# Performance work log

Hardware: AMD Instinct MI355X
Metric: run time of the kernel (lower is better)

The kernel has to match this reference:

```python
import jax, jax.numpy as jnp
import numpy as np

D = 32        # number of TT cores (d)
R = 16        # tt_rank
B = 262144    # batch size


def setup_inputs() -> dict:
    key = jax.random.key(0)
    k1, k2, k3, k4 = jax.random.split(key, 4)
    return {
        "X": jax.random.randint(k1, (B, D), 0, 2, dtype=jnp.int32),
        "core_first": jax.random.normal(k2, (1, R, 2), dtype=jnp.float32),
        "cores_mid": jax.random.normal(k3, (D - 2, R, R, 2), dtype=jnp.float32),
        "core_last": jax.random.normal(k4, (R, 1, 2), dtype=jnp.float32),
    }


def reference(X, core_first, cores_mid, core_last):
    # First core: cores[0][:, :, X[:,0]] -> [1, R, B] -> permute -> [B, 1, R].
    # We carry the squeezed [B, R] row vector instead of [B, 1, R].
    carry0 = jnp.take(core_first[0], X[:, 0], axis=-1).T  # [B, R]

    def step(carry, inp):
        core, idx = inp                       # core: [R, R, 2], idx: [B]
        c = jnp.take(core, idx, axis=2)       # gathered core: [R, R, B]
        new = jnp.einsum('br,rsb->bs', carry, c)  # batched (1xR)@(RxR)
        return new, None

    # Middle cores i = 1 .. D-2 (sequential chain, data-dependent).
    carry, _ = jax.lax.scan(step, carry0, (cores_mid, X[:, 1:D - 1].T))

    # Last core: cores[-1][:, :, X[:,-1]] -> [R, 1, B]; contract to scalar per batch.
    c_last = jnp.take(core_last[:, 0, :], X[:, -1], axis=-1)  # [R, B]
    out = jnp.einsum('br,rb->b', carry, c_last)               # [B]  (squeeze of [B,1,1])
    return out
```

## Files before the change

### kernel.cpp

```cpp
#include <hip/hip_runtime.h>


#define R 16
#define TT_D 32
#define BATCH 262144

#define OFF_V16  0
#define OFF_W16  1048576
#define OFF_P8   2097152
#define OFF_Q8   (OFF_P8 + 65536)
#define OFF_V8   (OFF_Q8 + 65536)
#define OFF_W8   (OFF_V8 + 4096)
#define OFF_PK   (OFF_W8 + 4096)
#define WS_FLOATS (OFF_PK + BATCH)

#define NBLK1 1024
#define NTAB  34

__device__ __forceinline__ void rowvec_mat(const float* __restrict__ M,
                                           float* __restrict__ u) {
    float nv[R];
    #pragma unroll
    for (int s = 0; s < R; s++) nv[s] = 0.f;
    #pragma unroll
    for (int t2 = 0; t2 < R; t2++) {
        const float a = u[t2];
        #pragma unroll
        for (int s = 0; s < R; s++) nv[s] += a * M[t2 * 16 + s];
    }
    #pragma unroll
    for (int s = 0; s < R; s++) u[s] = nv[s];
}

__device__ __forceinline__ void mat_colvec(const float* __restrict__ M,
                                           float* __restrict__ w) {
    float nw[R];
    #pragma unroll
    for (int r2 = 0; r2 < R; r2++) {
        float a = 0.f;
        #pragma unroll
        for (int k = 0; k < R; k++) a += M[r2 * 16 + k] * w[k];
        nw[r2] = a;
    }
    #pragma unroll
    for (int r2 = 0; r2 < R; r2++) w[r2] = nw[r2];
}

__global__ __launch_bounds__(256) void tt_stage1(const int* __restrict__ X,
                                                 const float* __restrict__ cf,
                                                 const float* __restrict__ cm,
                                                 const float* __restrict__ cl,
                                                 float* __restrict__ ws) {
    __shared__ float scm[8 * 512];
    const int blk = blockIdx.x;
    const int t = threadIdx.x;

    if (blk < NTAB) {
        int cbase, ncore;
        if (blk < 16)       { cbase = 7;  ncore = 8; }
        else if (blk < 32)  { cbase = 15; ncore = 8; }
        else if (blk == 32) { cbase = 0;  ncore = 7; }
        else                { cbase = 23; ncore = 7; }
        const float2* cm2 = (const float2*)(cm + cbase * 512);
        for (int j = t; j < ncore * 256; j += 256) {
            const float2 vv = cm2[j];
            const int ci = j >> 8, idx = j & 255;
            scm[ci * 512 + idx] = vv.x;
            scm[ci * 512 + 256 + idx] = vv.y;
        }
        __syncthreads();

        if (blk < 32) {
            const bool isP = (blk < 16);
            const int e = (isP ? blk : blk - 16) * 16 + (t >> 4), r = t & 15;
            float u[R];
            const float* M0 = scm + ((e >> 7) & 1) * 256;
            #pragma unroll
            for (int s = 0; s < R; s++) u[s] = M0[r * 16 + s];
            for (int k = 1; k < 8; k++)
                rowvec_mat(scm + k * 512 + ((e >> (7 - k)) & 1) * 256, u);
            float* o = ws + (isP ? OFF_P8 : OFF_Q8) + e * 256 + r * 16;
            #pragma unroll
            for (int s = 0; s < R; s++) o[s] = u[s];
        } else if (blk == 32) {
            const int e = t;
            float u[R];
            #pragma unroll
            for (int s = 0; s < R; s++) u[s] = cf[s * 2 + ((e >> 7) & 1)];
            for (int k = 0; k < 7; k++)
                rowvec_mat(scm + k * 512 + ((e >> (6 - k)) & 1) * 256, u);
            float* o = ws + OFF_V8 + e * 16;
            #pragma unroll
            for (int s = 0; s < R; s++) o[s] = u[s];
        } else {
            const int e = t;
            float w[R];
            #pragma unroll
            for (int r2 = 0; r2 < R; r2++) w[r2] = cl[r2 * 2 + (e & 1)];
            for (int j = 6; j >= 0; j--)
                mat_colvec(scm + j * 512 + ((e >> (7 - j)) & 1) * 256, w);
            float* o = ws + OFF_W8 + e * 16;
            #pragma unroll
            for (int r2 = 0; r2 < R; r2++) o[r2] = w[r2];
        }
    } else {
        unsigned* pk = (unsigned*)(ws + OFF_PK);
        const int stride = (NBLK1 - NTAB) * 256;
        for (int b = (blk - NTAB) * 256 + t; b < BATCH; b += stride) {
            const int4* Xr = (const int4*)(X + (size_t)b * TT_D);
            unsigned p = 0, s = 0;
            #pragma unroll
            for (int q = 0; q < 4; q++) {
                const int4 c = Xr[q];
                p = (p << 4) | ((unsigned)(c.x & 1) << 3) | ((unsigned)(c.y & 1) << 2)
                             | ((unsigned)(c.z & 1) << 1) | (unsigned)(c.w & 1);
            }
            #pragma unroll
            for (int q = 4; q < 8; q++) {
                const int4 c = Xr[q];
                s = (s << 4) | ((unsigned)(c.x & 1) << 3) | ((unsigned)(c.y & 1) << 2)
                             | ((unsigned)(c.z & 1) << 1) | (unsigned)(c.w & 1);
            }
            pk[b] = (p << 16) | s;
        }
    }
}

__global__ __launch_bounds__(256) void tt_stage2(float* __restrict__ ws) {
    __shared__ float sQ[256];
    const int blk = blockIdx.x;
    const int t = threadIdx.x;
    if (blk < 256) {
        const int hi = blk, lo = t;
        float u[R];
        const float* v8 = ws + OFF_V8 + hi * 16;
        #pragma unroll
        for (int k = 0; k < R; k++) u[k] = v8[k];
        rowvec_mat(ws + OFF_P8 + lo * 256, u);
        float* o = ws + OFF_V16 + (size_t)(hi * 256 + lo) * 16;
        #pragma unroll
        for (int s = 0; s < R; s++) o[s] = u[s];
    } else {
        const int hi = blk - 256, lo = t;
        sQ[t] = ws[OFF_Q8 + hi * 256 + t];
        __syncthreads();
        float w[R];
        const float* w8 = ws + OFF_W8 + lo * 16;
        #pragma unroll
        for (int k = 0; k < R; k++) w[k] = w8[k];
        mat_colvec(sQ, w);
        float* o = ws + OFF_W16 + (size_t)(hi * 256 + lo) * 16;
        #pragma unroll
        for (int r2 = 0; r2 < R; r2++) o[r2] = w[r2];
    }
}

__global__ __launch_bounds__(256) void tt_gather(const float* __restrict__ ws,
                                                 float* __restrict__ out) {
    const int b = blockIdx.x * 256 + threadIdx.x;
    const unsigned pk = ((const unsigned*)(ws + OFF_PK))[b];
    const unsigned p = pk >> 16, s = pk & 0xffffu;
    const float4* v = (const float4*)(ws + OFF_V16 + (size_t)p * 16);
    const float4* w = (const float4*)(ws + OFF_W16 + (size_t)s * 16);
    float acc = 0.f;
    #pragma unroll
    for (int k = 0; k < 4; k++) {
        const float4 a = v[k], c = w[k];
        acc += a.x * c.x + a.y * c.y + a.z * c.z + a.w * c.w;
    }
    out[b] = acc;
}

__global__ __launch_bounds__(256) void tt_direct(const int* __restrict__ X,
                                                 const float* __restrict__ cf,
                                                 const float* __restrict__ cm,
                                                 const float* __restrict__ cl,
                                                 float* __restrict__ out) {
    __shared__ float scm[30 * 16 * 16 * 2];
    for (int i = threadIdx.x; i < 30 * 16 * 16 * 2; i += blockDim.x) scm[i] = cm[i];
    __syncthreads();
    const int b = blockIdx.x * blockDim.x + threadIdx.x;
    if (b >= BATCH) return;
    const int* xr = X + (size_t)b * TT_D;
    float v[R], nv[R];
    const int x0 = xr[0] & 1;
    #pragma unroll
    for (int rr = 0; rr < R; rr++) v[rr] = cf[rr * 2 + x0];
    for (int i = 1; i <= 30; i++) {
        const int bit = xr[i] & 1;
        const float* M = scm + (i - 1) * 512;
        #pragma unroll
        for (int s2 = 0; s2 < R; s2++) {
            float acc = 0.f;
            #pragma unroll
            for (int rr = 0; rr < R; rr++) acc += v[rr] * M[(rr * 16 + s2) * 2 + bit];
            nv[s2] = acc;
        }
        #pragma unroll
        for (int s2 = 0; s2 < R; s2++) v[s2] = nv[s2];
    }
    const int xl = xr[31] & 1;
    float acc = 0.f;
    #pragma unroll
    for (int rr = 0; rr < R; rr++) acc += v[rr] * cl[rr * 2 + xl];
    out[b] = acc;
}

extern "C" void kernel_launch(void* const* d_in, const int* in_sizes, int n_in,
                              void* d_out, int out_size, void* d_ws, size_t ws_size,
                              hipStream_t stream) {
    const int* X = (const int*)d_in[0];
    const float* cf = (const float*)d_in[1];
    const float* cm = (const float*)d_in[2];
    const float* cl = (const float*)d_in[3];
    float* out = (float*)d_out;

    if (ws_size >= (size_t)WS_FLOATS * sizeof(float)) {
        float* ws = (float*)d_ws;
        tt_stage1<<<NBLK1, 256, 0, stream>>>(X, cf, cm, cl, ws);
        tt_stage2<<<512, 256, 0, stream>>>(ws);
        tt_gather<<<BATCH / 256, 256, 0, stream>>>(ws, out);
    } else {
        tt_direct<<<(BATCH + 255) / 256, 256, 0, stream>>>(X, cf, cm, cl, out);
    }
}
```

Baseline: 117.4 us.

## Replace three-kernel prefix/suffix table scheme with single direct per-row chain kernel

Removes the meet-in-the-middle scheme that built 65536-entry prefix and suffix tables, along with its stage kernels, workspace, and gather step. Each thread now packs its row of X into a 32-bit mask and runs the full 30-step 16x16 vector-matrix chain against cores held in shared memory. The cores are de-interleaved into shared memory so each matrix row reads contiguously. This drops two launches and the large workspace traffic, but costs about 30x more arithmetic per batch element, and every block reloads 60KB of cores into shared memory.

```diff
diff --git a/kernel.cpp b/kernel.cpp
--- a/kernel.cpp
+++ b/kernel.cpp
@@ -4,18 +4,6 @@
 #define R 16
 #define TT_D 32
 #define BATCH 262144
-
-#define OFF_V16  0
-#define OFF_W16  1048576
-#define OFF_P8   2097152
-#define OFF_Q8   (OFF_P8 + 65536)
-#define OFF_V8   (OFF_Q8 + 65536)
-#define OFF_W8   (OFF_V8 + 4096)
-#define OFF_PK   (OFF_W8 + 4096)
-#define WS_FLOATS (OFF_PK + BATCH)
-
-#define NBLK1 1024
-#define NTAB  34
 
 __device__ __forceinline__ void rowvec_mat(const float* __restrict__ M,
                                            float* __restrict__ u) {
@@ -32,177 +20,55 @@
     for (int s = 0; s < R; s++) u[s] = nv[s];
 }
 
-__device__ __forceinline__ void mat_colvec(const float* __restrict__ M,
-                                           float* __restrict__ w) {
-    float nw[R];
+__device__ __forceinline__ unsigned pack_elem(const int* __restrict__ X, int b) {
+    const int4* Xr = (const int4*)(X + (size_t)b * TT_D);
+    unsigned v = 0;
     #pragma unroll
-    for (int r2 = 0; r2 < R; r2++) {
-        float a = 0.f;
-        #pragma unroll
-        for (int k = 0; k < R; k++) a += M[r2 * 16 + k] * w[k];
-        nw[r2] = a;
+    for (int q = 0; q < 8; q++) {
+        const int4 c = Xr[q];
+        v = (v << 4) | ((unsigned)(c.x & 1) << 3) | ((unsigned)(c.y & 1) << 2)
+                     | ((unsigned)(c.z & 1) << 1) | (unsigned)(c.w & 1);
     }
-    #pragma unroll
-    for (int r2 = 0; r2 < R; r2++) w[r2] = nw[r2];
+    return v;
 }
 
-__global__ __launch_bounds__(256) void tt_stage1(const int* __restrict__ X,
-                                                 const float* __restrict__ cf,
-                                                 const float* __restrict__ cm,
-                                                 const float* __restrict__ cl,
-                                                 float* __restrict__ ws) {
-    __shared__ float scm[8 * 512];
-    const int blk = blockIdx.x;
+__global__ __launch_bounds__(256) void tt_chain(const int* __restrict__ X,
+                                                const float* __restrict__ cf,
+                                                const float* __restrict__ cm,
+                                                const float* __restrict__ cl,
+                                                float* __restrict__ out) {
+    __shared__ float scm[30 * 512];
     const int t = threadIdx.x;
 
-    if (blk < NTAB) {
-        int cbase, ncore;
-        if (blk < 16)       { cbase = 7;  ncore = 8; }
-        else if (blk < 32)  { cbase = 15; ncore = 8; }
-        else if (blk == 32) { cbase = 0;  ncore = 7; }
-        else                { cbase = 23; ncore = 7; }
-        const float2* cm2 = (const float2*)(cm + cbase * 512);
-        for (int j = t; j < ncore * 256; j += 256) {
+    {
+        const float2* cm2 = (const float2*)cm;
+        for (int j = t; j < 30 * 256; j += 256) {
             const float2 vv = cm2[j];
             const int ci = j >> 8, idx = j & 255;
             scm[ci * 512 + idx] = vv.x;
             scm[ci * 512 + 256 + idx] = vv.y;
         }
-        __syncthreads();
+    }
 
-        if (blk < 32) {
-            const bool isP = (blk < 16);
-            const int e = (isP ? blk : blk - 16) * 16 + (t >> 4), r = t & 15;
-            float u[R];
-            const float* M0 = scm + ((e >> 7) & 1) * 256;
-            #pragma unroll
-            for (int s = 0; s < R; s++) u[s] = M0[r * 16 + s];
-            for (int k = 1; k < 8; k++)
-                rowvec_mat(scm + k * 512 + ((e >> (7 - k)) & 1) * 256, u);
-            float* o = ws + (isP ? OFF_P8 : OFF_Q8) + e * 256 + r * 16;
-            #pragma unroll
-            for (int s = 0; s < R; s++) o[s] = u[s];
-        } else if (blk == 32) {
-            const int e = t;
-            float u[R];
-            #pragma unroll
-            for (int s = 0; s < R; s++) u[s] = cf[s * 2 + ((e >> 7) & 1)];
-            for (int k = 0; k < 7; k++)
-                rowvec_mat(scm + k * 512 + ((e >> (6 - k)) & 1) * 256, u);
-            float* o = ws + OFF_V8 + e * 16;
-            #pragma unroll
-            for (int s = 0; s < R; s++) o[s] = u[s];
-        } else {
-            const int e = t;
-            float w[R];
-            #pragma unroll
-            for (int r2 = 0; r2 < R; r2++) w[r2] = cl[r2 * 2 + (e & 1)];
-            for (int j = 6; j >= 0; j--)
-                mat_colvec(scm + j * 512 + ((e >> (7 - j)) & 1) * 256, w);
-            float* o = ws + OFF_W8 + e * 16;
-            #pragma unroll
-            for (int r2 = 0; r2 < R; r2++) o[r2] = w[r2];
-        }
-    } else {
-        unsigned* pk = (unsigned*)(ws + OFF_PK);
-        const int stride = (NBLK1 - NTAB) * 256;
-        for (int b = (blk - NTAB) * 256 + t; b < BATCH; b += stride) {
-            const int4* Xr = (const int4*)(X + (size_t)b * TT_D);
-            unsigned p = 0, s = 0;
-            #pragma unroll
-            for (int q = 0; q < 4; q++) {
-                const int4 c = Xr[q];
-                p = (p << 4) | ((unsigned)(c.x & 1) << 3) | ((unsigned)(c.y & 1) << 2)
-                             | ((unsigned)(c.z & 1) << 1) | (unsigned)(c.w & 1);
-            }
-            #pragma unroll
-            for (int q = 4; q < 8; q++) {
-                const int4 c = Xr[q];
-                s = (s << 4) | ((unsigned)(c.x & 1) << 3) | ((unsigned)(c.y & 1) << 2)
-                             | ((unsigned)(c.z & 1) << 1) | (unsigned)(c.w & 1);
-            }
-            pk[b] = (p << 16) | s;
-        }
+    const int b = blockIdx.x * 256 + t;
+    const unsigned bits = pack_elem(X, b);
+
+    __syncthreads();
+
+    float v[R];
+    const int x0 = (int)(bits >> 31);
+    #pragma unroll
+    for (int r = 0; r < R; r++) v[r] = cf[r * 2 + x0];
+
+    for (int i = 1; i <= 30; i++) {
+        const float* M = scm + (i - 1) * 512 + (((bits >> (31 - i)) & 1) << 8);
+        rowvec_mat(M, v);
     }
-}
 
-__global__ __launch_bounds__(256) void tt_stage2(float* __restrict__ ws) {
-    __shared__ float sQ[256];
-    const int blk = blockIdx.x;
-    const int t = threadIdx.x;
-    if (blk < 256) {
-        const int hi = blk, lo = t;
-        float u[R];
-        const float* v8 = ws + OFF_V8 + hi * 16;
-        #pragma unroll
-        for (int k = 0; k < R; k++) u[k] = v8[k];
-        rowvec_mat(ws + OFF_P8 + lo * 256, u);
-        float* o = ws + OFF_V16 + (size_t)(hi * 256 + lo) * 16;
-        #pragma unroll
-        for (int s = 0; s < R; s++) o[s] = u[s];
-    } else {
-        const int hi = blk - 256, lo = t;
-        sQ[t] = ws[OFF_Q8 + hi * 256 + t];
-        __syncthreads();
-        float w[R];
-        const float* w8 = ws + OFF_W8 + lo * 16;
-        #pragma unroll
-        for (int k = 0; k < R; k++) w[k] = w8[k];
-        mat_colvec(sQ, w);
-        float* o = ws + OFF_W16 + (size_t)(hi * 256 + lo) * 16;
-        #pragma unroll
-        for (int r2 = 0; r2 < R; r2++) o[r2] = w[r2];
-    }
-}
-
-__global__ __launch_bounds__(256) void tt_gather(const float* __restrict__ ws,
-                                                 float* __restrict__ out) {
-    const int b = blockIdx.x * 256 + threadIdx.x;
-    const unsigned pk = ((const unsigned*)(ws + OFF_PK))[b];
-    const unsigned p = pk >> 16, s = pk & 0xffffu;
-    const float4* v = (const float4*)(ws + OFF_V16 + (size_t)p * 16);
-    const float4* w = (const float4*)(ws + OFF_W16 + (size_t)s * 16);
+    const int xl = (int)(bits & 1);
     float acc = 0.f;
     #pragma unroll
-    for (int k = 0; k < 4; k++) {
-        const float4 a = v[k], c = w[k];
-        acc += a.x * c.x + a.y * c.y + a.z * c.z + a.w * c.w;
-    }
-    out[b] = acc;
-}
-
-__global__ __launch_bounds__(256) void tt_direct(const int* __restrict__ X,
-                                                 const float* __restrict__ cf,
-                                                 const float* __restrict__ cm,
-                                                 const float* __restrict__ cl,
-                                                 float* __restrict__ out) {
-    __shared__ float scm[30 * 16 * 16 * 2];
-    for (int i = threadIdx.x; i < 30 * 16 * 16 * 2; i += blockDim.x) scm[i] = cm[i];
-    __syncthreads();
-    const int b = blockIdx.x * blockDim.x + threadIdx.x;
-    if (b >= BATCH) return;
-    const int* xr = X + (size_t)b * TT_D;
-    float v[R], nv[R];
-    const int x0 = xr[0] & 1;
-    #pragma unroll
-    for (int rr = 0; rr < R; rr++) v[rr] = cf[rr * 2 + x0];
-    for (int i = 1; i <= 30; i++) {
-        const int bit = xr[i] & 1;
-        const float* M = scm + (i - 1) * 512;
-        #pragma unroll
-        for (int s2 = 0; s2 < R; s2++) {
-            float acc = 0.f;
-            #pragma unroll
-            for (int rr = 0; rr < R; rr++) acc += v[rr] * M[(rr * 16 + s2) * 2 + bit];
-            nv[s2] = acc;
-        }
-        #pragma unroll
-        for (int s2 = 0; s2 < R; s2++) v[s2] = nv[s2];
-    }
-    const int xl = xr[31] & 1;
-    float acc = 0.f;
-    #pragma unroll
-    for (int rr = 0; rr < R; rr++) acc += v[rr] * cl[rr * 2 + xl];
+    for (int r = 0; r < R; r++) acc += v[r] * cl[r * 2 + xl];
     out[b] = acc;
 }
 
@@ -214,13 +80,7 @@
     const float* cm = (const float*)d_in[2];
     const float* cl = (const float*)d_in[3];
     float* out = (float*)d_out;
+    (void)d_ws; (void)ws_size;
 
-    if (ws_size >= (size_t)WS_FLOATS * sizeof(float)) {
-        float* ws = (float*)d_ws;
-        tt_stage1<<<NBLK1, 256, 0, stream>>>(X, cf, cm, cl, ws);
-        tt_stage2<<<512, 256, 0, stream>>>(ws);
-        tt_gather<<<BATCH / 256, 256, 0, stream>>>(ws, out);
-    } else {
-        tt_direct<<<(BATCH + 255) / 256, 256, 0, stream>>>(X, cf, cm, cl, out);
-    }
+    tt_chain<<<BATCH / 256, 256, 0, stream>>>(X, cf, cm, cl, out);
 }
```

Measured after the change: 192.0 us. 63.5% more time.
